# Performance work log

Hardware: AMD Instinct MI355X
Metric: run time of the kernel (lower is better)

The kernel has to match this reference:

```python
import jax, jax.numpy as jnp
import numpy as np

CONF_THRES = 0.596
IOU_THRES = 0.45
MAX_WH = 4096.0
K_CAND = 512      # NMS candidate cap (static)
MAX_DET = 300     # padded detections per image
IMG = 768.0       # hw = x[1].shape[-2:] * 8 -> 96*8


def _bilinear(feat, y, x):
    # feat: [C,H,W]; y,x: [R,S] sample coords. torchvision-style bilinear w/ border handling.
    C, H, W = feat.shape
    valid = (y > -1.0) & (y < H) & (x > -1.0) & (x < W)
    y = jnp.clip(y, 0.0)
    x = jnp.clip(x, 0.0)
    y0 = jnp.minimum(jnp.floor(y), H - 1).astype(jnp.int32)
    x0 = jnp.minimum(jnp.floor(x), W - 1).astype(jnp.int32)
    y1 = jnp.minimum(y0 + 1, H - 1)
    x1 = jnp.minimum(x0 + 1, W - 1)
    ly = y - y0
    lx = x - x0
    hy = 1.0 - ly
    hx = 1.0 - lx
    f00 = feat[:, y0, x0]
    f01 = feat[:, y0, x1]
    f10 = feat[:, y1, x0]
    f11 = feat[:, y1, x1]
    val = hy * hx * f00 + hy * lx * f01 + ly * hx * f10 + ly * lx * f11
    return val * valid  # [C,R,S]


def _roi_align_1x1(feat, boxes, scale):
    # RoIAlign(output_size=1, aligned=False); adaptive sampling_ratio replaced by fixed 2x2 grid.
    b = boxes * scale
    x1, y1, x2, y2 = b[:, 0], b[:, 1], b[:, 2], b[:, 3]
    rw = jnp.maximum(x2 - x1, 1.0)
    rh = jnp.maximum(y2 - y1, 1.0)
    offs = jnp.array([0.25, 0.75], dtype=boxes.dtype)  # (i+0.5)/2
    ys = y1[:, None] + rh[:, None] * offs  # [R,2]
    xs = x1[:, None] + rw[:, None] * offs
    R = ys.shape[0]
    yy = jnp.broadcast_to(ys[:, :, None], (R, 2, 2)).reshape(R, 4)
    xx = jnp.broadcast_to(xs[:, None, :], (R, 2, 2)).reshape(R, 4)
    v = _bilinear(feat, yy, xx)  # [C,R,4]
    return v.mean(-1).T  # [R,C]


def _iou_matrix(b):
    area = (b[:, 2] - b[:, 0]) * (b[:, 3] - b[:, 1])
    lt = jnp.maximum(b[:, None, :2], b[None, :, :2])
    rb = jnp.minimum(b[:, None, 2:], b[None, :, 2:])
    wh = jnp.clip(rb - lt, 0.0)
    inter = wh[..., 0] * wh[..., 1]
    return inter / (area[:, None] + area[None, :] - inter + 1e-7)


def _nms_image(pred):
    # pred: [N, 5+nc]. yolov5 non_max_suppression, static-shape version.
    obj = pred[:, 4]
    conf_all = pred[:, 5:] * obj[:, None]
    conf = conf_all.max(-1)
    cls = jnp.argmax(conf_all, -1)
    xy = pred[:, :2]
    wh = pred[:, 2:4]
    boxes = jnp.concatenate([xy - wh / 2, xy + wh / 2], -1)  # xywh2xyxy
    valid = (obj > CONF_THRES) & (conf > CONF_THRES)
    score = jnp.where(valid, conf, 0.0)
    sc, idx = jax.lax.top_k(score, K_CAND)
    b = boxes[idx]
    c = cls[idx].astype(boxes.dtype)
    iou = _iou_matrix(b + c[:, None] * MAX_WH)  # per-class offset NMS
    ar = jnp.arange(K_CAND)

    def body(i, keep):
        sup = keep[i] & (iou[i] > IOU_THRES) & (ar > i)
        return keep & (~sup)

    keep = jax.lax.fori_loop(0, K_CAND, body, sc > 0.0)
    sc2 = jnp.where(keep, sc, 0.0)
    sc3, idx2 = jax.lax.top_k(sc2, MAX_DET)
    return b[idx2], sc3 > 0.0  # [MAX_DET,4], [MAX_DET]


def _per_image(pred, g1, g2, g3, g4, W1, b1, W2, b2):
    bbox, mask = _nms_image(pred)
    f = jnp.concatenate([
        _roi_align_1x1(g1, bbox, 1.0 / 8),
        _roi_align_1x1(g2, bbox, 1.0 / 16),
        _roi_align_1x1(g3, bbox, 1.0 / 32),
        _roi_align_1x1(g4, bbox, 1.0 / 64),
    ], axis=1)  # [MAX_DET, 1920]
    h = jax.nn.leaky_relu(f @ W1 + b1)
    h = jax.nn.leaky_relu(h @ W2 + b2)
    out = jnp.concatenate([bbox / IMG, h], axis=-1)  # [MAX_DET, 4+64]
    return out * mask[:, None].astype(out.dtype)


def setup_inputs() -> dict:
    key = jax.random.key(0)
    ks = jax.random.split(key, 9)
    B, N, NC = 8, 36720, 80
    r = jax.random.uniform(ks[0], (B, N, 5 + NC), dtype=jnp.float32)
    xy = r[..., :2] * IMG
    wh = r[..., 2:4] * 112.0 + 8.0
    preds = jnp.concatenate([xy, wh, r[..., 4:]], axis=-1)
    f1 = jax.random.normal(ks[1], (B, 128, 96, 96), dtype=jnp.float32)
    f2 = jax.random.normal(ks[2], (B, 256, 48, 48), dtype=jnp.float32)
    f3 = jax.random.normal(ks[3], (B, 512, 24, 24), dtype=jnp.float32)
    f4 = jax.random.normal(ks[4], (B, 1024, 12, 12), dtype=jnp.float32)
    W1 = jax.random.normal(ks[5], (1920, 64), dtype=jnp.float32) / np.sqrt(1920.0)
    b1 = jnp.zeros((64,), jnp.float32)
    W2 = jax.random.normal(ks[6], (64, 64), dtype=jnp.float32) / 8.0
    b2 = jnp.zeros((64,), jnp.float32)
    return {"preds": preds, "f1": f1, "f2": f2, "f3": f3, "f4": f4,
            "W1": W1, "b1": b1, "W2": W2, "b2": b2}


def reference(preds, f1, f2, f3, f4, W1, b1, W2, b2):
    fn = lambda p, a, b_, c, d: _per_image(p, a, b_, c, d, W1, b1, W2, b2)
    return jax.vmap(fn)(preds, f1, f2, f3, f4)  # [B, MAX_DET, 68]
```

## Files before the change

### kernel.cpp

```cpp
#include <hip/hip_runtime.h>
#include <cstdint>

#define B_IMG   8
#define NCAND   36720
#define PD      85
#define NCLS    80
#define KC      512
#define MAXDET  300
#define NBUCK   2048
#define CANDCAP 1024

#define G2_OFF 4718592
#define G3_OFF 5898240
#define G4_OFF 6193152
#define G_TOT  6266880

#define P2_BASE 0
#define P2_SLAB 1179648
#define P3_BASE 2359296
#define P3_SLAB 294912
#define P4_BASE 3538944
#define P4_SLAB 73728

typedef unsigned int u32;
typedef unsigned long long u64;

__device__ __forceinline__ float leaky(float x){ return x >= 0.f ? x : 0.01f*x; }

__device__ __forceinline__ u64 shfl_u64(u64 v, int lane){
  int lo = __shfl((int)(u32)(v & 0xFFFFFFFFull), lane, 64);
  int hi = __shfl((int)(u32)(v >> 32), lane, 64);
  return ((u64)(u32)hi << 32) | (u64)(u32)lo;
}
__device__ __forceinline__ u64 shfl_xor_u64(u64 v, int mask){
  int lo = __shfl_xor((int)(u32)(v & 0xFFFFFFFFull), mask, 64);
  int hi = __shfl_xor((int)(u32)(v >> 32), mask, 64);
  return ((u64)(u32)hi << 32) | (u64)(u32)lo;
}

__global__ __launch_bounds__(256) void k_score(const float* __restrict__ preds,
    u32* __restrict__ sbits, int* __restrict__ clsArr, u32* __restrict__ hist){
  __shared__ u32   sl_lane[4][64];
  __shared__ float sl_obj[4][64];
  __shared__ u32   sl_res[4][64];
  __shared__ u32   sl_cls[4][64];
  const int img  = blockIdx.y;
  const int wv   = threadIdx.x >> 6;
  const int lane = threadIdx.x & 63;
  const int base = (blockIdx.x*4 + wv)*64;
  const int ci   = base + lane;
  const bool inb = ci < NCAND;
  float obj = 0.f;
  if (inb) obj = preds[((long)img*NCAND + ci)*PD + 4];
  const bool pass = obj > 0.596f;
  u64 mask = __ballot(pass);
  int cnt  = __popcll(mask);
  int rank = __popcll(mask & ((1ull << lane) - 1ull));
  if (pass){ sl_lane[wv][rank] = (u32)lane; sl_obj[wv][rank] = obj; }
  const int q = lane & 3;
  for (int r0 = 0; r0 < cnt; r0 += 16){
    int idx = r0 + (lane >> 2);
    if (idx < cnt){
      u32 sl = sl_lane[wv][idx];
      float obj2 = sl_obj[wv][idx];
      const float* p2 = preds + ((long)img*NCAND + base + (int)sl)*PD + 5 + q;
      u64 best = 0ull;
      #pragma unroll
      for (int k = 0; k < 20; k++){
        float v = p2[4*k] * obj2;
        u64 key = ((u64)__float_as_uint(v) << 32) | (u64)(~(u32)(q + 4*k));
        if (key > best) best = key;
      }
      u64 o1 = shfl_xor_u64(best, 1); if (o1 > best) best = o1;
      u64 o2 = shfl_xor_u64(best, 2); if (o2 > best) best = o2;
      if (q == 0){
        u32 bits = (u32)(best >> 32);
        sl_res[wv][sl] = (__uint_as_float(bits) > 0.596f) ? bits : 0u;
        sl_cls[wv][sl] = ~(u32)(best & 0xFFFFFFFFull);
      }
    }
  }
  if (inb){
    u32 out = pass ? sl_res[wv][lane] : 0u;
    sbits[(long)img*NCAND + ci] = out;
    if (pass) clsArr[(long)img*NCAND + ci] = (int)sl_cls[wv][lane];
    if (out) atomicAdd(&hist[img*NBUCK + ((out - 0x3F000000u) >> 12)], 1u);
  }
}

__global__ __launch_bounds__(64) void k_thresh(const u32* __restrict__ hist,
                                               u32* __restrict__ thr){
  const int img = blockIdx.x;
  const int lane = threadIdx.x;
  const u32* h = hist + img*NBUCK;
  u32 acc = 0; u32 result = 0x3F000000u; bool found = false;
  for (int g = NBUCK/64 - 1; g >= 0 && !found; g--){
    u32 v = h[g*64 + lane];
    u32 s = v;
    #pragma unroll
    for (int off = 1; off < 64; off <<= 1){
      u32 t = __shfl_down(s, off, 64);
      s += (lane + off < 64) ? t : 0u;
    }
    u64 mask = __ballot(acc + s >= KC);
    if (mask){
      int hl = 63 - __clzll(mask);
      result = 0x3F000000u + ((u32)(g*64 + hl) << 12);
      found = true;
    }
    acc += __shfl(s, 0, 64);
  }
  if (lane == 0) thr[img] = result;
}

__global__ __launch_bounds__(256) void k_gather(const u32* __restrict__ sbits,
    const u32* __restrict__ thr, u32* __restrict__ cnt, u64* __restrict__ cand){
  int img = blockIdx.y;
  int n = blockIdx.x*256 + threadIdx.x;
  if (n >= NCAND) return;
  u32 bits = sbits[(long)img*NCAND + n];
  if (bits && bits >= thr[img]){
    u32 pos = atomicAdd(&cnt[img], 1u);
    if (pos < CANDCAP)
      cand[(long)img*CANDCAP + pos] = ((u64)bits << 32) | (u64)(0xFFFFFFFFu - (u32)n);
  }
}

__global__ __launch_bounds__(256) void k_rank(const float* __restrict__ preds,
    const int* __restrict__ clsArr, const u64* __restrict__ cand,
    const u32* __restrict__ cnt, float4* __restrict__ cbs_g,
    float4* __restrict__ obs_g, u64* __restrict__ kmask_g){
#pragma clang fp contract(off)
  __shared__ __align__(16) u64 keys[CANDCAP];
  const int img = blockIdx.x >> 2;
  const int sub = blockIdx.x & 3;
  const int tid = threadIdx.x;
  const int M = min((int)cnt[img], CANDCAP);
  #pragma unroll
  for (int k = 0; k < 4; k++){
    int s = k*256 + tid;
    keys[s] = (s < M) ? cand[(long)img*CANDCAP + s] : 0ull;
  }
  __syncthreads();
  const int slot = sub*256 + tid;
  u64 k0 = keys[slot];
  int r0 = 0;
  const ulonglong2* kv = (const ulonglong2*)keys;
  for (int j = 0; j < CANDCAP/2; j++){
    ulonglong2 kk = kv[j];
    r0 += (kk.x > k0) + (kk.y > k0);
  }
  if ((k0 >> 32) != 0ull && r0 < KC){
    u32 idxn = 0xFFFFFFFFu - (u32)(k0 & 0xFFFFFFFFull);
    const float* p = preds + ((long)img*NCAND + idxn)*PD;
    float cx = p[0], cy = p[1], w = p[2], h = p[3];
    float hw = w*0.5f, hh = h*0.5f;
    float X1 = cx-hw, Y1 = cy-hh, X2 = cx+hw, Y2 = cy+hh;
    float off = (float)clsArr[(long)img*NCAND + idxn] * 4096.0f;
    obs_g[(long)img*KC + r0] = make_float4(X1, Y1, X2, Y2);
    cbs_g[(long)img*KC + r0] = make_float4(X1+off, Y1+off, X2+off, Y2+off);
    atomicOr(&kmask_g[img*8 + (r0 >> 6)], 1ull << (r0 & 63));
  }
}

__global__ __launch_bounds__(512) void k_iou(const float4* __restrict__ cbs_g,
    const u64* __restrict__ kmask_g, u64* __restrict__ lrows_g){
#pragma clang fp contract(off)
  __shared__ __align__(16) float4 cbsL[8*65];
  const int img = blockIdx.x >> 3;
  const int ch  = blockIdx.x & 7;
  const int tid = threadIdx.x;
  if (tid < KC){
    u64 km = kmask_g[img*8 + (tid >> 6)];
    bool f = (km >> (tid & 63)) & 1ull;
    float4 v = f ? cbs_g[(long)img*KC + tid]
                 : make_float4(-4e8f, -4e8f, -4e8f, -4e8f);
    cbsL[(tid >> 6)*65 + (tid & 63)] = v;
  }
  __syncthreads();
  const int row = ch*64 + (tid >> 3);
  const int w   = tid & 7;
  float4 bi = cbsL[(row >> 6)*65 + (row & 63)];
  float areai = (bi.z - bi.x)*(bi.w - bi.y);
  u64 bits = 0ull;
  const int jbase = w*64;
  for (int b = 0; b < 64; b++){
    int j = jbase + b;
    if (j > row){
      float4 bj = cbsL[w*65 + b];
      float areaj = (bj.z - bj.x)*(bj.w - bj.y);
      float ltx = fmaxf(bi.x, bj.x), lty = fmaxf(bi.y, bj.y);
      float rbx = fminf(bi.z, bj.z), rby = fminf(bi.w, bj.w);
      float ww = fmaxf(rbx - ltx, 0.f);
      float hh = fmaxf(rby - lty, 0.f);
      float inter = ww*hh;
      float iou = inter / (areai + areaj - inter + 1e-7f);
      if (iou > 0.45f) bits |= (1ull << b);
    }
  }
  lrows_g[((long)img*KC + row)*8 + w] = bits;
}

__global__ __launch_bounds__(512) void k_greedy(const u64* __restrict__ lrows_g,
    const u64* __restrict__ kmask_g, const float4* __restrict__ obs_g,
    float* __restrict__ selbox, u32* __restrict__ selcnt){
  __shared__ __align__(16) u64 lrows[KC*8];
  __shared__ u64 keepw[8];
  const int img = blockIdx.x;
  const int tid = threadIdx.x;
  const ulonglong2* src = (const ulonglong2*)(lrows_g + (long)img*KC*8);
  ulonglong2* dst = (ulonglong2*)lrows;
  #pragma unroll
  for (int k = 0; k < 4; k++) dst[k*512 + tid] = src[k*512 + tid];
  __syncthreads();
  if (tid < 64){
    const int lane = tid;
    const int w = lane & 7;
    u64 kw_own = kmask_g[img*8 + w];
    for (int b = 0; b < 8; b++){
      u64 kwb = shfl_u64(kw_own, b);
      for (int g = 0; g < 8; g++){
        u64 rdec[8], rown[8];
        #pragma unroll
        for (int k = 0; k < 8; k++){
          int i = b*64 + g*8 + k;
          rdec[k] = lrows[i*8 + b];
          rown[k] = lrows[i*8 + w];
        }
        #pragma unroll
        for (int k = 0; k < 8; k++){
          int il = g*8 + k;
          if ((kwb >> il) & 1ull){
            kwb    &= ~rdec[k];
            kw_own &= ~rown[k];
          }
        }
      }
    }
    if (lane < 8) keepw[lane] = kw_own;
  }
  __syncthreads();
  {
    u64 kk[8];
    #pragma unroll
    for (int w = 0; w < 8; w++) kk[w] = keepw[w];
    const int s = tid;
    const int wi = s >> 6, bi = s & 63;
    bool kept = (kk[wi] >> bi) & 1ull;
    if (kept){
      int rank = 0;
      for (int w = 0; w < wi; w++) rank += __popcll(kk[w]);
      rank += __popcll(bi ? (kk[wi] & ((1ull << bi) - 1ull)) : 0ull);
      if (rank < MAXDET){
        float4 ob = obs_g[(long)img*KC + s];
        float* sb = selbox + ((long)img*MAXDET + rank)*4;
        sb[0]=ob.x; sb[1]=ob.y; sb[2]=ob.z; sb[3]=ob.w;
      }
    }
    if (tid == 0){
      int tot = 0;
      #pragma unroll
      for (int w = 0; w < 8; w++) tot += __popcll(kk[w]);
      selcnt[img] = (u32)min(tot, MAXDET);
    }
  }
}

__device__ __forceinline__ void gld16(const void* g, void* l){
  __builtin_amdgcn_global_load_lds((const __attribute__((address_space(1))) void*)g,
                                   (__attribute__((address_space(3))) void*)l, 16, 0, 0);
}

__device__ __forceinline__ void stage_chunk(const float4* __restrict__ feat4,
    const float4* __restrict__ W14, long fbase, int hw4, int px04, int Woff,
    int c0, int tid, float4* FsD, float4* WsD){
  const int wb = tid & ~63;
  #pragma unroll
  for (int k = 0; k < 4; k++){
    int s = tid + k*128; int c = s >> 5, q = s & 31;
    int pq = px04 + q; if (pq >= hw4) pq = hw4 - 1;
    gld16(feat4 + fbase + (long)(c0 + c)*hw4 + pq, FsD + k*128 + wb);
  }
  #pragma unroll
  for (int k = 0; k < 2; k++){
    int s = tid + k*128; int c = s >> 4, q = s & 15;
    gld16(W14 + (long)(Woff + c0 + c)*16 + q, WsD + k*128 + wb);
  }
}

#define FMA_Q(S, W, A) \
  A.x = fmaf(S, W.x, A.x); A.y = fmaf(S, W.y, A.y); \
  A.z = fmaf(S, W.z, A.z); A.w = fmaf(S, W.w, A.w);

__global__ __launch_bounds__(128) void k_proj(const float* __restrict__ f1,
    const float* __restrict__ f2, const float* __restrict__ f3,
    const float* __restrict__ f4, const float* __restrict__ W1,
    float* __restrict__ G, float* __restrict__ P){
  __shared__ __align__(16) float Fs[2][16*128];
  __shared__ __align__(16) float Ws[2][16*64];
  const int img = blockIdx.y;
  const int u   = blockIdx.x;
  const float* feat; int C, HW, Woff, tile, split; long pbase; bool multi;
  if (u < 16)      { feat=f4; C=1024; HW=144;  Woff=896; tile=u>>3;      split=u&7;
                     pbase=P4_BASE + (long)split*P4_SLAB; multi=true;  }
  else if (u < 36) { feat=f3; C=512;  HW=576;  Woff=384; tile=(u-16)>>2; split=(u-16)&3;
                     pbase=P3_BASE + (long)split*P3_SLAB; multi=true;  }
  else if (u < 72) { feat=f2; C=256;  HW=2304; Woff=128; tile=(u-36)>>1; split=(u-36)&1;
                     pbase=P2_BASE + (long)split*P2_SLAB; multi=true;  }
  else             { feat=f1; C=128;  HW=9216; Woff=0;   tile=u-72;      split=0;
                     pbase=0; multi=false; }
  const int px0  = tile*128;
  const int hw4  = HW >> 2;
  const int px04 = px0 >> 2;
  const int tid  = threadIdx.x;
  const int jg   = tid & 7;
  const int pg   = tid >> 3;
  const int c0b  = split*128;
  const float4* feat4 = (const float4*)feat;
  const float4* W14   = (const float4*)W1;
  const long fbase = (long)img*C*hw4;
  float4 z = make_float4(0.f,0.f,0.f,0.f);
  float4 aA0=z,aA1=z,aA2=z,aA3=z,aA4=z,aA5=z,aA6=z,aA7=z;
  float4 aB0=z,aB1=z,aB2=z,aB3=z,aB4=z,aB5=z,aB6=z,aB7=z;

  stage_chunk(feat4, W14, fbase, hw4, px04, Woff, c0b, tid,
              (float4*)Fs[0], (float4*)Ws[0]);
  __syncthreads();
  for (int ch = 0; ch < 8; ch++){
    if (ch < 7)
      stage_chunk(feat4, W14, fbase, hw4, px04, Woff, c0b + (ch+1)*16, tid,
                  (float4*)Fs[(ch+1)&1], (float4*)Ws[(ch+1)&1]);
    const float4* fsb = (const float4*)Fs[ch&1];
    const float4* wsb = (const float4*)Ws[ch&1];
    #pragma unroll 4
    for (int c = 0; c < 16; c++){
      float4 fa = fsb[c*32 + pg*2];
      float4 fb = fsb[c*32 + pg*2 + 1];
      float4 wa = wsb[c*16 + jg*2];
      float4 wb = wsb[c*16 + jg*2 + 1];
      FMA_Q(fa.x, wa, aA0) FMA_Q(fa.y, wa, aA1) FMA_Q(fa.z, wa, aA2) FMA_Q(fa.w, wa, aA3)
      FMA_Q(fb.x, wa, aA4) FMA_Q(fb.y, wa, aA5) FMA_Q(fb.z, wa, aA6) FMA_Q(fb.w, wa, aA7)
      FMA_Q(fa.x, wb, aB0) FMA_Q(fa.y, wb, aB1) FMA_Q(fa.z, wb, aB2) FMA_Q(fa.w, wb, aB3)
      FMA_Q(fb.x, wb, aB4) FMA_Q(fb.y, wb, aB5) FMA_Q(fb.z, wb, aB6) FMA_Q(fb.w, wb, aB7)
    }
    __syncthreads();
  }
  float* outb = multi ? (P + pbase + (long)img*HW*64)
                      : (G + (long)img*HW*64);
  const int pxa = px0 + pg*8;
#define STOREQ(A, B, PP) do { int gp = pxa + (PP); if (gp < HW){ \
    *(float4*)(outb + (long)gp*64 + jg*8) = A; \
    *(float4*)(outb + (long)gp*64 + jg*8 + 4) = B; } } while(0)
  STOREQ(aA0, aB0, 0); STOREQ(aA1, aB1, 1); STOREQ(aA2, aB2, 2); STOREQ(aA3, aB3, 3);
  STOREQ(aA4, aB4, 4); STOREQ(aA5, aB5, 5); STOREQ(aA6, aB6, 6); STOREQ(aA7, aB7, 7);
#undef STOREQ
}

__global__ __launch_bounds__(256) void k_reduce(const float4* __restrict__ P4f,
                                                float4* __restrict__ G4f){
  const int N2 = P2_SLAB/4;
  const int N3 = P3_SLAB/4;
  const int N4 = P4_SLAB/4;
  int t = blockIdx.x*256 + threadIdx.x;
  if (t < N2){
    float4 a = P4f[t];
    float4 b = P4f[N2 + t];
    float4 r = make_float4(a.x+b.x, a.y+b.y, a.z+b.z, a.w+b.w);
    G4f[G2_OFF/4 + t] = r;
  } else if (t < N2 + N3){
    int u = t - N2;
    const float4* base = P4f + P3_BASE/4 + u;
    float4 r = base[0];
    #pragma unroll
    for (int s = 1; s < 4; s++){
      float4 b = base[(long)s*N3];
      r.x += b.x; r.y += b.y; r.z += b.z; r.w += b.w;
    }
    G4f[G3_OFF/4 + u] = r;
  } else if (t < N2 + N3 + N4){
    int u = t - N2 - N3;
    const float4* base = P4f + P4_BASE/4 + u;
    float4 r = base[0];
    #pragma unroll
    for (int s = 1; s < 8; s++){
      float4 b = base[(long)s*N4];
      r.x += b.x; r.y += b.y; r.z += b.z; r.w += b.w;
    }
    G4f[G4_OFF/4 + u] = r;
  }
}

__device__ __forceinline__ void roi_level(const float* __restrict__ g,
    int Hl, int Wl, float scale, float x1, float y1, float x2, float y2,
    int lane, float& h){
  float bx1=x1*scale, by1=y1*scale, bx2=x2*scale, by2=y2*scale;
  float rw=fmaxf(bx2-bx1,1.f), rh=fmaxf(by2-by1,1.f);
  float ys[2]={by1+rh*0.25f, by1+rh*0.75f};
  float xs[2]={bx1+rw*0.25f, bx1+rw*0.75f};
  #pragma unroll
  for (int pt = 0; pt < 4; pt++){
    float y=ys[pt>>1], x=xs[pt&1];
    if ((y>-1.f)&&(y<(float)Hl)&&(x>-1.f)&&(x<(float)Wl)){
      float yc=fmaxf(y,0.f), xc=fmaxf(x,0.f);
      int y0=(int)fminf(floorf(yc),(float)(Hl-1));
      int x0=(int)fminf(floorf(xc),(float)(Wl-1));
      int y1i=min(y0+1,Hl-1), x1i=min(x0+1,Wl-1);
      float ly=yc-(float)y0, lx=xc-(float)x0;
      float hy=1.f-ly, hx=1.f-lx;
      h += (hy*hx*0.25f)*g[(long)(y0*Wl+x0)*64+lane];
      h += (hy*lx*0.25f)*g[(long)(y0*Wl+x1i)*64+lane];
      h += (ly*hx*0.25f)*g[(long)(y1i*Wl+x0)*64+lane];
      h += (ly*lx*0.25f)*g[(long)(y1i*Wl+x1i)*64+lane];
    }
  }
}

__global__ __launch_bounds__(256) void k_roi_mlp(const float* __restrict__ G,
    const float* __restrict__ selbox, const u32* __restrict__ selcnt,
    const float* __restrict__ b1, const float* __restrict__ W2,
    const float* __restrict__ b2, float* __restrict__ out){
  const int img  = blockIdx.y;
  const int wave = threadIdx.x >> 6;
  const int lane = threadIdx.x & 63;
  const int slot = blockIdx.x*4 + wave;
  if (slot >= MAXDET) return;
  float* o = out + ((long)img*MAXDET + slot)*68;
  if (slot >= (int)selcnt[img]){
    o[4+lane] = 0.f;
    if (lane < 4) o[lane] = 0.f;
    return;
  }
  const float* sb = selbox + ((long)img*MAXDET + slot)*4;
  float x1 = sb[0], y1 = sb[1], x2 = sb[2], y2 = sb[3];
  const float* Gi1 = G +          (long)img*9216*64;
  const float* Gi2 = G + G2_OFF + (long)img*2304*64;
  const float* Gi3 = G + G3_OFF + (long)img*576*64;
  const float* Gi4 = G + G4_OFF + (long)img*144*64;
  float h = 0.f;
  roi_level(Gi1, 96, 96, 0.125f,    x1,y1,x2,y2, lane, h);
  roi_level(Gi2, 48, 48, 0.0625f,   x1,y1,x2,y2, lane, h);
  roi_level(Gi3, 24, 24, 0.03125f,  x1,y1,x2,y2, lane, h);
  roi_level(Gi4, 12, 12, 0.015625f, x1,y1,x2,y2, lane, h);
  float h1 = leaky(h + b1[lane]);
  float c = 0.f;
  #pragma unroll 8
  for (int k = 0; k < 64; k++){
    float hk = __shfl(h1, k, 64);
    c += hk * W2[k*64 + lane];
  }
  o[4+lane] = leaky(c + b2[lane]);
  if (lane < 4) o[lane] = sb[lane] / 768.0f;
}

#define WS_G 2914048
#define WS_P 27981568

extern "C" void kernel_launch(void* const* d_in, const int* in_sizes, int n_in,
                              void* d_out, int out_size, void* d_ws, size_t ws_size,
                              hipStream_t stream){
  const float* preds = (const float*)d_in[0];
  const float* f1 = (const float*)d_in[1];
  const float* f2 = (const float*)d_in[2];
  const float* f3 = (const float*)d_in[3];
  const float* f4 = (const float*)d_in[4];
  const float* W1 = (const float*)d_in[5];
  const float* b1 = (const float*)d_in[6];
  const float* W2 = (const float*)d_in[7];
  const float* b2 = (const float*)d_in[8];
  float* out = (float*)d_out;
  char* ws = (char*)d_ws;
  u32* hist    = (u32*)(ws + 0);
  u32* cnt     = (u32*)(ws + 65536);
  u64* kmask_g = (u64*)(ws + 65792);
  u32* thr     = (u32*)(ws + 66304);
  float* selb  = (float*)(ws + 66560);
  u32* selc    = (u32*)(ws + 104960);
  u32* sbits   = (u32*)(ws + 105216);
  int* clsA    = (int*)(ws + 1280256);
  u64* cand    = (u64*)(ws + 2455296);
  float4* cbs_g = (float4*)(ws + 2520832);
  float4* obs_g = (float4*)(ws + 2586368);
  u64* lrows_g  = (u64*)(ws + 2651904);
  float* G     = (float*)(ws + WS_G);
  float* P     = (float*)(ws + WS_P);

  hipMemsetAsync(ws, 0, 66304, stream);

  dim3 gs((NCAND + 255)/256, B_IMG);
  k_score<<<gs, 256, 0, stream>>>(preds, sbits, clsA, hist);
  k_thresh<<<B_IMG, 64, 0, stream>>>(hist, thr);
  dim3 g3((NCAND+255)/256, B_IMG);
  k_gather<<<g3, 256, 0, stream>>>(sbits, thr, cnt, cand);
  k_rank<<<B_IMG*4, 256, 0, stream>>>(preds, clsA, cand, cnt, cbs_g, obs_g, kmask_g);
  k_iou<<<B_IMG*8, 512, 0, stream>>>(cbs_g, kmask_g, lrows_g);
  k_greedy<<<B_IMG, 512, 0, stream>>>(lrows_g, kmask_g, obs_g, selb, selc);
  k_proj<<<dim3(144, B_IMG), 128, 0, stream>>>(f1, f2, f3, f4, W1, G, P);
  k_reduce<<<1512, 256, 0, stream>>>((const float4*)P, (float4*)G);
  k_roi_mlp<<<dim3((MAXDET+3)/4, B_IMG), 256, 0, stream>>>(G, selb, selc, b1, W2, b2, out);
}
```

Baseline: 327.9 us.

## Merge score and feature projection into one launch; fold reduce into rank kernel

New measurement: 328.2 us. About the same (+0.1%).

```diff
diff --git a/kernel.cpp b/kernel.cpp
--- a/kernel.cpp
+++ b/kernel.cpp
@@ -38,54 +38,147 @@
   return ((u64)(u32)hi << 32) | (u64)(u32)lo;
 }
 
-__global__ __launch_bounds__(256) void k_score(const float* __restrict__ preds,
-    u32* __restrict__ sbits, int* __restrict__ clsArr, u32* __restrict__ hist){
-  __shared__ u32   sl_lane[4][64];
-  __shared__ float sl_obj[4][64];
-  __shared__ u32   sl_res[4][64];
-  __shared__ u32   sl_cls[4][64];
-  const int img  = blockIdx.y;
-  const int wv   = threadIdx.x >> 6;
-  const int lane = threadIdx.x & 63;
-  const int base = (blockIdx.x*4 + wv)*64;
-  const int ci   = base + lane;
-  const bool inb = ci < NCAND;
-  float obj = 0.f;
-  if (inb) obj = preds[((long)img*NCAND + ci)*PD + 4];
-  const bool pass = obj > 0.596f;
-  u64 mask = __ballot(pass);
-  int cnt  = __popcll(mask);
-  int rank = __popcll(mask & ((1ull << lane) - 1ull));
-  if (pass){ sl_lane[wv][rank] = (u32)lane; sl_obj[wv][rank] = obj; }
-  const int q = lane & 3;
-  for (int r0 = 0; r0 < cnt; r0 += 16){
-    int idx = r0 + (lane >> 2);
-    if (idx < cnt){
-      u32 sl = sl_lane[wv][idx];
-      float obj2 = sl_obj[wv][idx];
-      const float* p2 = preds + ((long)img*NCAND + base + (int)sl)*PD + 5 + q;
-      u64 best = 0ull;
-      #pragma unroll
-      for (int k = 0; k < 20; k++){
-        float v = p2[4*k] * obj2;
-        u64 key = ((u64)__float_as_uint(v) << 32) | (u64)(~(u32)(q + 4*k));
-        if (key > best) best = key;
+__device__ __forceinline__ void gld16(const void* g, void* l){
+  __builtin_amdgcn_global_load_lds((const __attribute__((address_space(1))) void*)g,
+                                   (__attribute__((address_space(3))) void*)l, 16, 0, 0);
+}
+
+__device__ __forceinline__ void stage8(const float4* __restrict__ feat4,
+    const float4* __restrict__ W14, long fbase, int hw4, int px04, int Woff,
+    int c0, int tid, float4* FsD, float4* WsD){
+  const int wb = tid & ~63;
+  #pragma unroll
+  for (int k = 0; k < 2; k++){
+    int s = tid + k*256; int c = s >> 6, q = s & 63;
+    int pq = px04 + q; if (pq >= hw4) pq = hw4 - 1;
+    gld16(feat4 + fbase + (long)(c0 + c)*hw4 + pq, FsD + k*256 + wb);
+  }
+  if (tid < 128){
+    int c = tid >> 4, q = tid & 15;
+    gld16(W14 + (long)(Woff + c0 + c)*16 + q, WsD + wb);
+  }
+}
+
+#define FMA_Q(S, W, A) \
+  A.x = fmaf(S, W.x, A.x); A.y = fmaf(S, W.y, A.y); \
+  A.z = fmaf(S, W.z, A.z); A.w = fmaf(S, W.w, A.w);
+
+__global__ __launch_bounds__(256) void k_front(const float* __restrict__ preds,
+    u32* __restrict__ sbits, int* __restrict__ clsArr, u32* __restrict__ hist,
+    const float* __restrict__ f1, const float* __restrict__ f2,
+    const float* __restrict__ f3, const float* __restrict__ f4,
+    const float* __restrict__ W1, float* __restrict__ G, float* __restrict__ P){
+  __shared__ __align__(16) float smem[5120];
+  const int img = blockIdx.y;
+  const int u   = blockIdx.x;
+  const int tid = threadIdx.x;
+
+  if (u < 144){
+    u32*   sl_lane = (u32*)smem;
+    float* sl_obj  = smem + 256;
+    u32*   sl_res  = (u32*)(smem + 512);
+    u32*   sl_cls  = (u32*)(smem + 768);
+    const int wv   = tid >> 6;
+    const int lane = tid & 63;
+    const int base = (u*4 + wv)*64;
+    const int ci   = base + lane;
+    const bool inb = ci < NCAND;
+    float obj = 0.f;
+    if (inb) obj = preds[((long)img*NCAND + ci)*PD + 4];
+    const bool pass = obj > 0.596f;
+    u64 mask = __ballot(pass);
+    int cnt  = __popcll(mask);
+    int rank = __popcll(mask & ((1ull << lane) - 1ull));
+    if (pass){ sl_lane[wv*64 + rank] = (u32)lane; sl_obj[wv*64 + rank] = obj; }
+    const int q = lane & 3;
+    for (int r0 = 0; r0 < cnt; r0 += 16){
+      int idx = r0 + (lane >> 2);
+      if (idx < cnt){
+        u32 sl = sl_lane[wv*64 + idx];
+        float obj2 = sl_obj[wv*64 + idx];
+        const float* p2 = preds + ((long)img*NCAND + base + (int)sl)*PD + 5 + q;
+        u64 best = 0ull;
+        #pragma unroll
+        for (int k = 0; k < 20; k++){
+          float v = p2[4*k] * obj2;
+          u64 key = ((u64)__float_as_uint(v) << 32) | (u64)(~(u32)(q + 4*k));
+          if (key > best) best = key;
+        }
+        u64 o1 = shfl_xor_u64(best, 1); if (o1 > best) best = o1;
+        u64 o2 = shfl_xor_u64(best, 2); if (o2 > best) best = o2;
+        if (q == 0){
+          u32 bits = (u32)(best >> 32);
+          sl_res[wv*64 + sl] = (__uint_as_float(bits) > 0.596f) ? bits : 0u;
+          sl_cls[wv*64 + sl] = ~(u32)(best & 0xFFFFFFFFull);
+        }
       }
-      u64 o1 = shfl_xor_u64(best, 1); if (o1 > best) best = o1;
-      u64 o2 = shfl_xor_u64(best, 2); if (o2 > best) best = o2;
-      if (q == 0){
-        u32 bits = (u32)(best >> 32);
-        sl_res[wv][sl] = (__uint_as_float(bits) > 0.596f) ? bits : 0u;
-        sl_cls[wv][sl] = ~(u32)(best & 0xFFFFFFFFull);
-      }
-    }
-  }
-  if (inb){
-    u32 out = pass ? sl_res[wv][lane] : 0u;
-    sbits[(long)img*NCAND + ci] = out;
-    if (pass) clsArr[(long)img*NCAND + ci] = (int)sl_cls[wv][lane];
-    if (out) atomicAdd(&hist[img*NBUCK + ((out - 0x3F000000u) >> 12)], 1u);
-  }
+    }
+    if (inb){
+      u32 out = pass ? sl_res[wv*64 + lane] : 0u;
+      sbits[(long)img*NCAND + ci] = out;
+      if (pass) clsArr[(long)img*NCAND + ci] = (int)sl_cls[wv*64 + lane];
+      if (out) atomicAdd(&hist[img*NBUCK + ((out - 0x3F000000u) >> 12)], 1u);
+    }
+    return;
+  }
+
+  float4* Fs0 = (float4*)smem;
+  float4* Fs1 = Fs0 + 512;
+  float4* Ws0 = Fs0 + 1024;
+  float4* Ws1 = Fs0 + 1152;
+  const int v = u - 144;
+  const float* feat; int C, HW, Woff, tile, split; long pbase; bool multi;
+  if (v < 8)       { feat=f4; C=1024; HW=144;  Woff=896; tile=0;         split=v;
+                     pbase=P4_BASE + (long)split*P4_SLAB; multi=true;  }
+  else if (v < 20) { feat=f3; C=512;  HW=576;  Woff=384; tile=(v-8)>>2;  split=(v-8)&3;
+                     pbase=P3_BASE + (long)split*P3_SLAB; multi=true;  }
+  else if (v < 38) { feat=f2; C=256;  HW=2304; Woff=128; tile=(v-20)>>1; split=(v-20)&1;
+                     pbase=P2_BASE + (long)split*P2_SLAB; multi=true;  }
+  else             { feat=f1; C=128;  HW=9216; Woff=0;   tile=v-38;      split=0;
+                     pbase=0; multi=false; }
+  const int px0  = tile*256;
+  const int hw4  = HW >> 2;
+  const int px04 = px0 >> 2;
+  const int jg   = tid & 7;
+  const int pg   = tid >> 3;
+  const int c0b  = split*128;
+  const float4* feat4 = (const float4*)feat;
+  const float4* W14   = (const float4*)W1;
+  const long fbase = (long)img*C*hw4;
+  float4 z = make_float4(0.f,0.f,0.f,0.f);
+  float4 aA0=z,aA1=z,aA2=z,aA3=z,aA4=z,aA5=z,aA6=z,aA7=z;
+  float4 aB0=z,aB1=z,aB2=z,aB3=z,aB4=z,aB5=z,aB6=z,aB7=z;
+
+  stage8(feat4, W14, fbase, hw4, px04, Woff, c0b, tid, Fs0, Ws0);
+  __syncthreads();
+  for (int ch = 0; ch < 16; ch++){
+    if (ch < 15)
+      stage8(feat4, W14, fbase, hw4, px04, Woff, c0b + (ch+1)*8, tid,
+             (ch & 1) ? Fs0 : Fs1, (ch & 1) ? Ws0 : Ws1);
+    const float4* fsb = (ch & 1) ? Fs1 : Fs0;
+    const float4* wsb = (ch & 1) ? Ws1 : Ws0;
+    #pragma unroll
+    for (int c = 0; c < 8; c++){
+      float4 fa = fsb[c*64 + pg*2];
+      float4 fb = fsb[c*64 + pg*2 + 1];
+      float4 wa = wsb[c*16 + jg*2];
+      float4 wc = wsb[c*16 + jg*2 + 1];
+      FMA_Q(fa.x, wa, aA0) FMA_Q(fa.y, wa, aA1) FMA_Q(fa.z, wa, aA2) FMA_Q(fa.w, wa, aA3)
+      FMA_Q(fb.x, wa, aA4) FMA_Q(fb.y, wa, aA5) FMA_Q(fb.z, wa, aA6) FMA_Q(fb.w, wa, aA7)
+      FMA_Q(fa.x, wc, aB0) FMA_Q(fa.y, wc, aB1) FMA_Q(fa.z, wc, aB2) FMA_Q(fa.w, wc, aB3)
+      FMA_Q(fb.x, wc, aB4) FMA_Q(fb.y, wc, aB5) FMA_Q(fb.z, wc, aB6) FMA_Q(fb.w, wc, aB7)
+    }
+    __syncthreads();
+  }
+  float* outb = multi ? (P + pbase + (long)img*HW*64)
+                      : (G + (long)img*HW*64);
+  const int pxa = px0 + pg*8;
+#define STOREQ(A, B, PP) do { int gp = pxa + (PP); if (gp < HW){ \
+    *(float4*)(outb + (long)gp*64 + jg*8) = A; \
+    *(float4*)(outb + (long)gp*64 + jg*8 + 4) = B; } } while(0)
+  STOREQ(aA0, aB0, 0); STOREQ(aA1, aB1, 1); STOREQ(aA2, aB2, 2); STOREQ(aA3, aB3, 3);
+  STOREQ(aA4, aB4, 4); STOREQ(aA5, aB5, 5); STOREQ(aA6, aB6, 6); STOREQ(aA7, aB7, 7);
+#undef STOREQ
 }
 
 __global__ __launch_bounds__(64) void k_thresh(const u32* __restrict__ hist,
@@ -126,40 +219,75 @@
   }
 }
 
-__global__ __launch_bounds__(256) void k_rank(const float* __restrict__ preds,
+__global__ __launch_bounds__(256) void k_mid(const float* __restrict__ preds,
     const int* __restrict__ clsArr, const u64* __restrict__ cand,
     const u32* __restrict__ cnt, float4* __restrict__ cbs_g,
-    float4* __restrict__ obs_g, u64* __restrict__ kmask_g){
+    float4* __restrict__ obs_g, u64* __restrict__ kmask_g,
+    const float4* __restrict__ P4f, float4* __restrict__ G4f){
 #pragma clang fp contract(off)
   __shared__ __align__(16) u64 keys[CANDCAP];
-  const int img = blockIdx.x >> 2;
-  const int sub = blockIdx.x & 3;
+  const int u   = blockIdx.x;
   const int tid = threadIdx.x;
-  const int M = min((int)cnt[img], CANDCAP);
-  #pragma unroll
-  for (int k = 0; k < 4; k++){
-    int s = k*256 + tid;
-    keys[s] = (s < M) ? cand[(long)img*CANDCAP + s] : 0ull;
-  }
-  __syncthreads();
-  const int slot = sub*256 + tid;
-  u64 k0 = keys[slot];
-  int r0 = 0;
-  const ulonglong2* kv = (const ulonglong2*)keys;
-  for (int j = 0; j < CANDCAP/2; j++){
-    ulonglong2 kk = kv[j];
-    r0 += (kk.x > k0) + (kk.y > k0);
-  }
-  if ((k0 >> 32) != 0ull && r0 < KC){
-    u32 idxn = 0xFFFFFFFFu - (u32)(k0 & 0xFFFFFFFFull);
-    const float* p = preds + ((long)img*NCAND + idxn)*PD;
-    float cx = p[0], cy = p[1], w = p[2], h = p[3];
-    float hw = w*0.5f, hh = h*0.5f;
-    float X1 = cx-hw, Y1 = cy-hh, X2 = cx+hw, Y2 = cy+hh;
-    float off = (float)clsArr[(long)img*NCAND + idxn] * 4096.0f;
-    obs_g[(long)img*KC + r0] = make_float4(X1, Y1, X2, Y2);
-    cbs_g[(long)img*KC + r0] = make_float4(X1+off, Y1+off, X2+off, Y2+off);
-    atomicOr(&kmask_g[img*8 + (r0 >> 6)], 1ull << (r0 & 63));
+  if (u < 32){
+    const int img = u >> 2;
+    const int sub = u & 3;
+    const int M = min((int)cnt[img], CANDCAP);
+    #pragma unroll
+    for (int k = 0; k < 4; k++){
+      int s = k*256 + tid;
+      keys[s] = (s < M) ? cand[(long)img*CANDCAP + s] : 0ull;
+    }
+    __syncthreads();
+    const int slot = sub*256 + tid;
+    u64 k0 = keys[slot];
+    int r0 = 0;
+    const ulonglong2* kv = (const ulonglong2*)keys;
+    for (int j = 0; j < CANDCAP/2; j++){
+      ulonglong2 kk = kv[j];
+      r0 += (kk.x > k0) + (kk.y > k0);
+    }
+    if ((k0 >> 32) != 0ull && r0 < KC){
+      u32 idxn = 0xFFFFFFFFu - (u32)(k0 & 0xFFFFFFFFull);
+      const float* p = preds + ((long)img*NCAND + idxn)*PD;
+      float cx = p[0], cy = p[1], w = p[2], h = p[3];
+      float hw = w*0.5f, hh = h*0.5f;
+      float X1 = cx-hw, Y1 = cy-hh, X2 = cx+hw, Y2 = cy+hh;
+      float off = (float)clsArr[(long)img*NCAND + idxn] * 4096.0f;
+      obs_g[(long)img*KC + r0] = make_float4(X1, Y1, X2, Y2);
+      cbs_g[(long)img*KC + r0] = make_float4(X1+off, Y1+off, X2+off, Y2+off);
+      atomicOr(&kmask_g[img*8 + (r0 >> 6)], 1ull << (r0 & 63));
+    }
+    return;
+  }
+  const int N2 = P2_SLAB/4;
+  const int N3 = P3_SLAB/4;
+  const int N4 = P4_SLAB/4;
+  int t = (u - 32)*256 + tid;
+  if (t < N2){
+    float4 a = P4f[t];
+    float4 b = P4f[N2 + t];
+    float4 r = make_float4(a.x+b.x, a.y+b.y, a.z+b.z, a.w+b.w);
+    G4f[G2_OFF/4 + t] = r;
+  } else if (t < N2 + N3){
+    int w = t - N2;
+    const float4* base = P4f + P3_BASE/4 + w;
+    float4 r = base[0];
+    #pragma unroll
+    for (int s = 1; s < 4; s++){
+      float4 b = base[(long)s*N3];
+      r.x += b.x; r.y += b.y; r.z += b.z; r.w += b.w;
+    }
+    G4f[G3_OFF/4 + w] = r;
+  } else if (t < N2 + N3 + N4){
+    int w = t - N2 - N3;
+    const float4* base = P4f + P4_BASE/4 + w;
+    float4 r = base[0];
+    #pragma unroll
+    for (int s = 1; s < 8; s++){
+      float4 b = base[(long)s*N4];
+      r.x += b.x; r.y += b.y; r.z += b.z; r.w += b.w;
+    }
+    G4f[G4_OFF/4 + w] = r;
   }
 }
 
@@ -266,130 +394,6 @@
   }
 }
 
-__device__ __forceinline__ void gld16(const void* g, void* l){
-  __builtin_amdgcn_global_load_lds((const __attribute__((address_space(1))) void*)g,
-                                   (__attribute__((address_space(3))) void*)l, 16, 0, 0);
-}
-
-__device__ __forceinline__ void stage_chunk(const float4* __restrict__ feat4,
-    const float4* __restrict__ W14, long fbase, int hw4, int px04, int Woff,
-    int c0, int tid, float4* FsD, float4* WsD){
-  const int wb = tid & ~63;
-  #pragma unroll
-  for (int k = 0; k < 4; k++){
-    int s = tid + k*128; int c = s >> 5, q = s & 31;
-    int pq = px04 + q; if (pq >= hw4) pq = hw4 - 1;
-    gld16(feat4 + fbase + (long)(c0 + c)*hw4 + pq, FsD + k*128 + wb);
-  }
-  #pragma unroll
-  for (int k = 0; k < 2; k++){
-    int s = tid + k*128; int c = s >> 4, q = s & 15;
-    gld16(W14 + (long)(Woff + c0 + c)*16 + q, WsD + k*128 + wb);
-  }
-}
-
-#define FMA_Q(S, W, A) \
-  A.x = fmaf(S, W.x, A.x); A.y = fmaf(S, W.y, A.y); \
-  A.z = fmaf(S, W.z, A.z); A.w = fmaf(S, W.w, A.w);
-
-__global__ __launch_bounds__(128) void k_proj(const float* __restrict__ f1,
-    const float* __restrict__ f2, const float* __restrict__ f3,
-    const float* __restrict__ f4, const float* __restrict__ W1,
-    float* __restrict__ G, float* __restrict__ P){
-  __shared__ __align__(16) float Fs[2][16*128];
-  __shared__ __align__(16) float Ws[2][16*64];
-  const int img = blockIdx.y;
-  const int u   = blockIdx.x;
-  const float* feat; int C, HW, Woff, tile, split; long pbase; bool multi;
-  if (u < 16)      { feat=f4; C=1024; HW=144;  Woff=896; tile=u>>3;      split=u&7;
-                     pbase=P4_BASE + (long)split*P4_SLAB; multi=true;  }
-  else if (u < 36) { feat=f3; C=512;  HW=576;  Woff=384; tile=(u-16)>>2; split=(u-16)&3;
-                     pbase=P3_BASE + (long)split*P3_SLAB; multi=true;  }
-  else if (u < 72) { feat=f2; C=256;  HW=2304; Woff=128; tile=(u-36)>>1; split=(u-36)&1;
-                     pbase=P2_BASE + (long)split*P2_SLAB; multi=true;  }
-  else             { feat=f1; C=128;  HW=9216; Woff=0;   tile=u-72;      split=0;
-                     pbase=0; multi=false; }
-  const int px0  = tile*128;
-  const int hw4  = HW >> 2;
-  const int px04 = px0 >> 2;
-  const int tid  = threadIdx.x;
-  const int jg   = tid & 7;
-  const int pg   = tid >> 3;
-  const int c0b  = split*128;
-  const float4* feat4 = (const float4*)feat;
-  const float4* W14   = (const float4*)W1;
-  const long fbase = (long)img*C*hw4;
-  float4 z = make_float4(0.f,0.f,0.f,0.f);
-  float4 aA0=z,aA1=z,aA2=z,aA3=z,aA4=z,aA5=z,aA6=z,aA7=z;
-  float4 aB0=z,aB1=z,aB2=z,aB3=z,aB4=z,aB5=z,aB6=z,aB7=z;
-
-  stage_chunk(feat4, W14, fbase, hw4, px04, Woff, c0b, tid,
-              (float4*)Fs[0], (float4*)Ws[0]);
-  __syncthreads();
-  for (int ch = 0; ch < 8; ch++){
-    if (ch < 7)
-      stage_chunk(feat4, W14, fbase, hw4, px04, Woff, c0b + (ch+1)*16, tid,
-                  (float4*)Fs[(ch+1)&1], (float4*)Ws[(ch+1)&1]);
-    const float4* fsb = (const float4*)Fs[ch&1];
-    const float4* wsb = (const float4*)Ws[ch&1];
-    #pragma unroll 4
-    for (int c = 0; c < 16; c++){
-      float4 fa = fsb[c*32 + pg*2];
-      float4 fb = fsb[c*32 + pg*2 + 1];
-      float4 wa = wsb[c*16 + jg*2];
-      float4 wb = wsb[c*16 + jg*2 + 1];
-      FMA_Q(fa.x, wa, aA0) FMA_Q(fa.y, wa, aA1) FMA_Q(fa.z, wa, aA2) FMA_Q(fa.w, wa, aA3)
-      FMA_Q(fb.x, wa, aA4) FMA_Q(fb.y, wa, aA5) FMA_Q(fb.z, wa, aA6) FMA_Q(fb.w, wa, aA7)
-      FMA_Q(fa.x, wb, aB0) FMA_Q(fa.y, wb, aB1) FMA_Q(fa.z, wb, aB2) FMA_Q(fa.w, wb, aB3)
-      FMA_Q(fb.x, wb, aB4) FMA_Q(fb.y, wb, aB5) FMA_Q(fb.z, wb, aB6) FMA_Q(fb.w, wb, aB7)
-    }
-    __syncthreads();
-  }
-  float* outb = multi ? (P + pbase + (long)img*HW*64)
-                      : (G + (long)img*HW*64);
-  const int pxa = px0 + pg*8;
-#define STOREQ(A, B, PP) do { int gp = pxa + (PP); if (gp < HW){ \
-    *(float4*)(outb + (long)gp*64 + jg*8) = A; \
-    *(float4*)(outb + (long)gp*64 + jg*8 + 4) = B; } } while(0)
-  STOREQ(aA0, aB0, 0); STOREQ(aA1, aB1, 1); STOREQ(aA2, aB2, 2); STOREQ(aA3, aB3, 3);
-  STOREQ(aA4, aB4, 4); STOREQ(aA5, aB5, 5); STOREQ(aA6, aB6, 6); STOREQ(aA7, aB7, 7);
-#undef STOREQ
-}
-
-__global__ __launch_bounds__(256) void k_reduce(const float4* __restrict__ P4f,
-                                                float4* __restrict__ G4f){
-  const int N2 = P2_SLAB/4;
-  const int N3 = P3_SLAB/4;
-  const int N4 = P4_SLAB/4;
-  int t = blockIdx.x*256 + threadIdx.x;
-  if (t < N2){
-    float4 a = P4f[t];
-    float4 b = P4f[N2 + t];
-    float4 r = make_float4(a.x+b.x, a.y+b.y, a.z+b.z, a.w+b.w);
-    G4f[G2_OFF/4 + t] = r;
-  } else if (t < N2 + N3){
-    int u = t - N2;
-    const float4* base = P4f + P3_BASE/4 + u;
-    float4 r = base[0];
-    #pragma unroll
-    for (int s = 1; s < 4; s++){
-      float4 b = base[(long)s*N3];
-      r.x += b.x; r.y += b.y; r.z += b.z; r.w += b.w;
-    }
-    G4f[G3_OFF/4 + u] = r;
-  } else if (t < N2 + N3 + N4){
-    int u = t - N2 - N3;
-    const float4* base = P4f + P4_BASE/4 + u;
-    float4 r = base[0];
-    #pragma unroll
-    for (int s = 1; s < 8; s++){
-      float4 b = base[(long)s*N4];
-      r.x += b.x; r.y += b.y; r.z += b.z; r.w += b.w;
-    }
-    G4f[G4_OFF/4 + u] = r;
-  }
-}
-
 __device__ __forceinline__ void roi_level(const float* __restrict__ g,
     int Hl, int Wl, float scale, float x1, float y1, float x2, float y2,
     int lane, float& h){
@@ -486,15 +490,13 @@
 
   hipMemsetAsync(ws, 0, 66304, stream);
 
-  dim3 gs((NCAND + 255)/256, B_IMG);
-  k_score<<<gs, 256, 0, stream>>>(preds, sbits, clsA, hist);
+  k_front<<<dim3(218, B_IMG), 256, 0, stream>>>(preds, sbits, clsA, hist,
+                                                f1, f2, f3, f4, W1, G, P);
   k_thresh<<<B_IMG, 64, 0, stream>>>(hist, thr);
-  dim3 g3((NCAND+255)/256, B_IMG);
-  k_gather<<<g3, 256, 0, stream>>>(sbits, thr, cnt, cand);
-  k_rank<<<B_IMG*4, 256, 0, stream>>>(preds, clsA, cand, cnt, cbs_g, obs_g, kmask_g);
+  k_gather<<<dim3(144, B_IMG), 256, 0, stream>>>(sbits, thr, cnt, cand);
+  k_mid<<<32 + 1512, 256, 0, stream>>>(preds, clsA, cand, cnt, cbs_g, obs_g,
+                                       kmask_g, (const float4*)P, (float4*)G);
   k_iou<<<B_IMG*8, 512, 0, stream>>>(cbs_g, kmask_g, lrows_g);
   k_greedy<<<B_IMG, 512, 0, stream>>>(lrows_g, kmask_g, obs_g, selb, selc);
-  k_proj<<<dim3(144, B_IMG), 128, 0, stream>>>(f1, f2, f3, f4, W1, G, P);
-  k_reduce<<<1512, 256, 0, stream>>>((const float4*)P, (float4*)G);
-  k_roi_mlp<<<dim3((MAXDET+3)/4, B_IMG), 256, 0, stream>>>(G, selb, selc, b1, W2, b2, out);
-}
+  k_roi_mlp<<<dim3(75, B_IMG), 256, 0, stream>>>(G, selb, selc, b1, W2, b2, out);
+}
```
